# Performance work log

Measured on AMD Instinct MI355X. Metric: run time of the kernel, lower is better.

The kernel has to match this reference:

```python
import jax, jax.numpy as jnp
import numpy as np

B, N, FIN = 4, 4096, 128
H, U = 4, 32

def setup_inputs() -> dict:
    key = jax.random.key(0)
    k = jax.random.split(key, 6)
    x = jax.random.normal(k[0], (B, N, FIN), dtype=jnp.float32)
    adj = (jax.random.uniform(k[1], (B, N, N)) < 0.05).astype(jnp.float32)
    glorot = lambda kk, shape, fi, fo: jax.random.uniform(kk, shape, jnp.float32,
                                                          -np.sqrt(6.0/(fi+fo)), np.sqrt(6.0/(fi+fo)))
    W = glorot(k[2], (FIN, H*U), FIN, H*U)
    a_src = glorot(k[3], (H, U, 1), U, 1)
    a_dst = glorot(k[4], (H, U, 1), U, 1)
    bias = jnp.zeros((H*U,), dtype=jnp.float32)
    return {"x": x, "adj": adj, "W": W, "a_src": a_src, "a_dst": a_dst, "bias": bias}

def reference(x, adj, W, a_src, a_dst, bias):
    # inference mode: attention dropout is a no-op
    b, n, _ = x.shape
    h_heads, u = a_src.shape[0], a_src.shape[1]
    # add self-loops, clip to {0,1}
    adj = jnp.clip(adj + jnp.eye(n, dtype=adj.dtype)[None], 0.0, 1.0)
    h = (x @ W).reshape(b, n, h_heads, u).transpose(0, 2, 1, 3)      # [B,H,N,U]
    f1 = jnp.einsum('bhnu,hu->bhn', h, a_src[..., 0])                # [B,H,N]
    f2 = jnp.einsum('bhnu,hu->bhn', h, a_dst[..., 0])                # [B,H,N]
    e = f1[:, :, :, None] + f2[:, :, None, :]                        # [B,H,N,N]
    e = jnp.where(e > 0, e, 0.2 * e)                                 # LeakyReLU(0.2)
    e = jnp.where(adj[:, None] > 0.0, e, jnp.float32(-1e9))
    alpha = jax.nn.softmax(e, axis=-1)
    out = jnp.einsum('bhij,bhju->bhiu', alpha, h)                    # [B,H,N,U]
    out = out.transpose(0, 2, 1, 3).reshape(b, n, h_heads * u) + bias
    return jnp.where(out > 0, out, jnp.expm1(out))                   # ELU
```

## Files before the change

kernel.cpp:

```cpp
#include <hip/hip_runtime.h>
#include <math.h>

#define NB   4
#define NN   4096
#define FIN  128
#define FOUT 128
#define NH   4
#define UU   32

__device__ __forceinline__ unsigned short f2bf(float f) {
    unsigned u = __float_as_uint(f);
    u += 0x7fff + ((u >> 16) & 1);
    return (unsigned short)(u >> 16);
}

#define K1_ROWS 64
#define K1_RT   8
#define K1_CT   4
#define XPAD    132

__global__ __launch_bounds__(256) void k1_feat(
    const float* __restrict__ x, const float* __restrict__ W,
    const float* __restrict__ a_src, const float* __restrict__ a_dst,
    unsigned short* __restrict__ hbf, float* __restrict__ f1g, float* __restrict__ f2g)
{
    __shared__ __align__(16) float Wq[32 * FOUT];
    __shared__ __align__(16) float xs[K1_ROWS * XPAD];

    const int tid  = threadIdx.x;
    const int row0 = blockIdx.x * K1_ROWS;

    const float4* x4 = (const float4*)(x + (size_t)row0 * FIN);
    for (int idx = tid; idx < K1_ROWS * FIN / 4; idx += 256) {
        int r = idx >> 5, q = idx & 31;
        *(float4*)(xs + r * XPAD + q * 4) = x4[idx];
    }

    const int cg = tid & 31;
    const int rg = tid >> 5;
    float acc[K1_RT][K1_CT];
    #pragma unroll
    for (int rr = 0; rr < K1_RT; rr++)
        #pragma unroll
        for (int cc = 0; cc < K1_CT; cc++) acc[rr][cc] = 0.f;

    for (int kt = 0; kt < 4; kt++) {
        __syncthreads();
        for (int idx = tid; idx < 32 * FOUT / 4; idx += 256)
            ((float4*)Wq)[idx] = ((const float4*)W)[kt * 1024 + idx];
        __syncthreads();
        #pragma unroll
        for (int k4 = 0; k4 < 8; k4++) {
            const int kb = kt * 32 + k4 * 4;
            float4 xv[K1_RT];
            #pragma unroll
            for (int rr = 0; rr < K1_RT; rr++)
                xv[rr] = *(const float4*)(xs + (rg * K1_RT + rr) * XPAD + kb);
            #pragma unroll
            for (int kk = 0; kk < 4; kk++) {
                float wv[K1_CT];
                #pragma unroll
                for (int cc = 0; cc < K1_CT; cc++)
                    wv[cc] = Wq[(k4 * 4 + kk) * FOUT + cg + 32 * cc];
                #pragma unroll
                for (int rr = 0; rr < K1_RT; rr++) {
                    float xk = ((const float*)&xv[rr])[kk];
                    #pragma unroll
                    for (int cc = 0; cc < K1_CT; cc++)
                        acc[rr][cc] = fmaf(xk, wv[cc], acc[rr][cc]);
                }
            }
        }
    }
    __syncthreads();
    #pragma unroll
    for (int rr = 0; rr < K1_RT; rr++)
        #pragma unroll
        for (int cc = 0; cc < K1_CT; cc++)
            xs[(rg * K1_RT + rr) * XPAD + cg + 32 * cc] = acc[rr][cc];
    __syncthreads();

    unsigned short* hrow = hbf + (size_t)row0 * FOUT;
    for (int idx = tid; idx < K1_ROWS * FOUT / 8; idx += 256) {
        int r = idx >> 4, q = idx & 15;
        const float* src = xs + r * XPAD + q * 8;
        uint4 o;
        o.x = (unsigned)f2bf(src[0]) | ((unsigned)f2bf(src[1]) << 16);
        o.y = (unsigned)f2bf(src[2]) | ((unsigned)f2bf(src[3]) << 16);
        o.z = (unsigned)f2bf(src[4]) | ((unsigned)f2bf(src[5]) << 16);
        o.w = (unsigned)f2bf(src[6]) | ((unsigned)f2bf(src[7]) << 16);
        *(uint4*)(hrow + (size_t)r * FOUT + q * 8) = o;
    }

    for (int task = tid; task < K1_ROWS * NH * 2; task += 256) {
        int row = task >> 3;
        int head = (task >> 1) & 3;
        int which = task & 1;
        const float* av = which ? a_dst : a_src;
        float s = 0.f;
        #pragma unroll
        for (int u = 0; u < UU; u++)
            s += xs[row * XPAD + head * UU + u] * av[head * UU + u];
        float* dst = which ? f2g : f1g;
        dst[(size_t)(row0 + row) * NH + head] = s;
    }
}

#define CAP   512
#define APAD  516
#define PPART 132

__device__ __forceinline__ float lrelu(float e) { return e > 0.f ? e : 0.2f * e; }

__global__ __launch_bounds__(256) void k2_gat(
    const float* __restrict__ adj, const unsigned short* __restrict__ hbf,
    const float* __restrict__ f1g, const float* __restrict__ f2g,
    const float* __restrict__ bias, float* __restrict__ out)
{
    const int q    = blockIdx.x;
    const int xcd  = q & 7;
    const int b    = xcd >> 1;
    const int i    = ((q >> 3) << 1) | (xcd & 1);
    const int row  = b * NN + i;
    const int tid  = threadIdx.x;
    const int lane = tid & 63;
    const int wv   = tid >> 6;

    __shared__ int   nbr[CAP];
    __shared__ float alpha[NH][APAD];
    __shared__ float part[16][PPART];
    __shared__ float inv_s[NH];
    __shared__ int   wcnt[4];

    const float4* arow = (const float4*)(adj + (size_t)row * NN);
    float4 v[4];
    #pragma unroll
    for (int it = 0; it < 4; it++)
        v[it] = arow[wv * 256 + it * 64 + lane];

    const unsigned long long below = (1ull << lane) - 1ull;
    int my_cnt = 0;
    #pragma unroll
    for (int it = 0; it < 4; it++) {
        const int jb = (wv * 256 + it * 64 + lane) << 2;
        my_cnt += __popcll(__ballot((v[it].x > 0.f) | (jb + 0 == i)));
        my_cnt += __popcll(__ballot((v[it].y > 0.f) | (jb + 1 == i)));
        my_cnt += __popcll(__ballot((v[it].z > 0.f) | (jb + 2 == i)));
        my_cnt += __popcll(__ballot((v[it].w > 0.f) | (jb + 3 == i)));
    }
    if (lane == 0) wcnt[wv] = my_cnt;
    __syncthreads();

    const int w0 = wcnt[0], w1 = wcnt[1], w2 = wcnt[2], w3 = wcnt[3];
    int run = (wv > 0 ? w0 : 0) + (wv > 1 ? w1 : 0) + (wv > 2 ? w2 : 0);
    const int total = w0 + w1 + w2 + w3;
    const int K = (total < CAP) ? total : CAP;

    const float4* f2b = (const float4*)(f2g + (size_t)b * NN * NH);
    const float4  f1v = ((const float4*)f1g)[row];
    #pragma unroll
    for (int it = 0; it < 4; it++) {
        const int jb = (wv * 256 + it * 64 + lane) << 2;
        const bool p0 = (v[it].x > 0.f) | (jb + 0 == i);
        const bool p1 = (v[it].y > 0.f) | (jb + 1 == i);
        const bool p2 = (v[it].z > 0.f) | (jb + 2 == i);
        const bool p3 = (v[it].w > 0.f) | (jb + 3 == i);
        unsigned long long m0 = __ballot(p0), m1 = __ballot(p1);
        unsigned long long m2 = __ballot(p2), m3 = __ballot(p3);
        int c0 = __popcll(m0), c1 = __popcll(m1), c2 = __popcll(m2), c3 = __popcll(m3);
        #pragma unroll
        for (int e = 0; e < 4; e++) {
            bool pe = e == 0 ? p0 : e == 1 ? p1 : e == 2 ? p2 : p3;
            unsigned long long me = e == 0 ? m0 : e == 1 ? m1 : e == 2 ? m2 : m3;
            int pre = e == 0 ? 0 : e == 1 ? c0 : e == 2 ? c0 + c1 : c0 + c1 + c2;
            if (pe) {
                int p = run + pre + __popcll(me & below);
                if (p < CAP) {
                    int j = jb + e;
                    nbr[p] = j;
                    float4 f2v = f2b[j];
                    alpha[0][p] = lrelu(f1v.x + f2v.x);
                    alpha[1][p] = lrelu(f1v.y + f2v.y);
                    alpha[2][p] = lrelu(f1v.z + f2v.z);
                    alpha[3][p] = lrelu(f1v.w + f2v.w);
                }
            }
        }
        run += c0 + c1 + c2 + c3;
    }
    __syncthreads();

    {
        float m = -1e30f;
        for (int k = lane; k < K; k += 64) m = fmaxf(m, alpha[wv][k]);
        #pragma unroll
        for (int off = 32; off > 0; off >>= 1) m = fmaxf(m, __shfl_xor(m, off, 64));
        float s = 0.f;
        for (int k = lane; k < K; k += 64) {
            float a = __expf(alpha[wv][k] - m);
            alpha[wv][k] = a;
            s += a;
        }
        #pragma unroll
        for (int off = 32; off > 0; off >>= 1) s += __shfl_xor(s, off, 64);
        if (lane == 0) inv_s[wv] = 1.f / s;
    }
    __syncthreads();

    const int cq = tid & 15;
    const int kg = tid >> 4;
    const int hh = cq >> 2;
    const unsigned short* hb = hbf + (size_t)b * NN * FOUT + cq * 8;
    float acc[8];
    #pragma unroll
    for (int t = 0; t < 8; t++) acc[t] = 0.f;

    int k = kg;
    for (; k + 16 < K; k += 32) {
        int j0 = nbr[k], j1 = nbr[k + 16];
        float a0 = alpha[hh][k], a1 = alpha[hh][k + 16];
        uint4 u4a = *(const uint4*)(hb + (size_t)j0 * FOUT);
        uint4 u4b = *(const uint4*)(hb + (size_t)j1 * FOUT);
        const unsigned* u0 = (const unsigned*)&u4a;
        const unsigned* u1 = (const unsigned*)&u4b;
        #pragma unroll
        for (int t = 0; t < 4; t++) {
            acc[2*t]   = fmaf(a0, __uint_as_float(u0[t] << 16),          acc[2*t]);
            acc[2*t+1] = fmaf(a0, __uint_as_float(u0[t] & 0xffff0000u),  acc[2*t+1]);
        }
        #pragma unroll
        for (int t = 0; t < 4; t++) {
            acc[2*t]   = fmaf(a1, __uint_as_float(u1[t] << 16),          acc[2*t]);
            acc[2*t+1] = fmaf(a1, __uint_as_float(u1[t] & 0xffff0000u),  acc[2*t+1]);
        }
    }
    if (k < K) {
        int j0 = nbr[k];
        float a0 = alpha[hh][k];
        uint4 u4a = *(const uint4*)(hb + (size_t)j0 * FOUT);
        const unsigned* u0 = (const unsigned*)&u4a;
        #pragma unroll
        for (int t = 0; t < 4; t++) {
            acc[2*t]   = fmaf(a0, __uint_as_float(u0[t] << 16),          acc[2*t]);
            acc[2*t+1] = fmaf(a0, __uint_as_float(u0[t] & 0xffff0000u),  acc[2*t+1]);
        }
    }
    *(float4*)&part[kg][cq * 8]     = *(float4*)&acc[0];
    *(float4*)&part[kg][cq * 8 + 4] = *(float4*)&acc[4];
    __syncthreads();

    if (tid < FOUT) {
        float o = 0.f;
        #pragma unroll
        for (int g = 0; g < 16; g++) o += part[g][tid];
        o = o * inv_s[tid >> 5] + bias[tid];
        o = o > 0.f ? o : expm1f(o);
        out[(size_t)row * FOUT + tid] = o;
    }
}

extern "C" void kernel_launch(void* const* d_in, const int* in_sizes, int n_in,
                              void* d_out, int out_size, void* d_ws, size_t ws_size,
                              hipStream_t stream) {
    const float* x     = (const float*)d_in[0];
    const float* adj   = (const float*)d_in[1];
    const float* W     = (const float*)d_in[2];
    const float* a_src = (const float*)d_in[3];
    const float* a_dst = (const float*)d_in[4];
    const float* bias  = (const float*)d_in[5];
    float* out = (float*)d_out;

    char* ws = (char*)d_ws;
    unsigned short* hbf = (unsigned short*)ws;
    float* f1g = (float*)(ws + (size_t)NB * NN * FOUT * 2);
    float* f2g = f1g + (size_t)NB * NN * NH;

    k1_feat<<<NB * NN / K1_ROWS, 256, 0, stream>>>(x, W, a_src, a_dst, hbf, f1g, f2g);
    k2_gat<<<NB * NN, 256, 0, stream>>>(adj, hbf, f1g, f2g, bias, out);
}
```

Baseline: 427.6 us.

## Process eight rows per block with register prefetch of next adjacency row

The GAT aggregation kernel now has each block loop over eight rows, strided by 512, instead of handling one row. The next row's adjacency slice and f1 values are loaded into registers while the current row is being processed, so the large adjacency read overlaps with compute. The softmax is reorganised so all 256 threads score neighbours for all four heads at once using float4 values, with cross-wave max and sum reductions in shared memory. Barriers become raw s_barrier calls that wait only on LDS. The trade-offs are higher register pressure from the prefetch buffers and a grid that fills the device only once, leaving less block-level parallelism to hide latency.

```diff
diff --git a/kernel.cpp b/kernel.cpp
--- a/kernel.cpp
+++ b/kernel.cpp
@@ -13,6 +13,8 @@
     u += 0x7fff + ((u >> 16) & 1);
     return (unsigned short)(u >> 16);
 }
+
+#define LBAR() asm volatile("s_waitcnt lgkmcnt(0)\n\ts_barrier" ::: "memory")
 
 #define K1_ROWS 64
 #define K1_RT   8
@@ -107,155 +109,206 @@
 }
 
 #define CAP   512
-#define APAD  516
 #define PPART 132
+#define RPB   8
 
 __device__ __forceinline__ float lrelu(float e) { return e > 0.f ? e : 0.2f * e; }
 
-__global__ __launch_bounds__(256) void k2_gat(
+__global__ __launch_bounds__(256, 8) void k2_gat(
     const float* __restrict__ adj, const unsigned short* __restrict__ hbf,
     const float* __restrict__ f1g, const float* __restrict__ f2g,
     const float* __restrict__ bias, float* __restrict__ out)
 {
-    const int q    = blockIdx.x;
-    const int xcd  = q & 7;
+    const int p    = blockIdx.x;
+    const int xcd  = p & 7;
     const int b    = xcd >> 1;
-    const int i    = ((q >> 3) << 1) | (xcd & 1);
-    const int row  = b * NN + i;
+    const int l    = ((p >> 3) << 1) | (p & 1);
     const int tid  = threadIdx.x;
     const int lane = tid & 63;
     const int wv   = tid >> 6;
 
-    __shared__ int   nbr[CAP];
-    __shared__ float alpha[NH][APAD];
-    __shared__ float part[16][PPART];
-    __shared__ float inv_s[NH];
-    __shared__ int   wcnt[4];
-
-    const float4* arow = (const float4*)(adj + (size_t)row * NN);
-    float4 v[4];
-    #pragma unroll
-    for (int it = 0; it < 4; it++)
-        v[it] = arow[wv * 256 + it * 64 + lane];
-
+    __shared__ int    nbr[CAP];
+    __shared__ __align__(16) float4 alpha4[CAP];
+    __shared__ float  part[16][PPART];
+    __shared__ __align__(16) float4 smax4[4];
+    __shared__ float  wsum[16];
+    __shared__ int    wcnt[4];
+
+    const float4* f2b = (const float4*)(f2g + (size_t)b * NN * NH);
+    const unsigned short* hbase = hbf + (size_t)b * NN * FOUT;
     const unsigned long long below = (1ull << lane) - 1ull;
-    int my_cnt = 0;
-    #pragma unroll
-    for (int it = 0; it < 4; it++) {
-        const int jb = (wv * 256 + it * 64 + lane) << 2;
-        my_cnt += __popcll(__ballot((v[it].x > 0.f) | (jb + 0 == i)));
-        my_cnt += __popcll(__ballot((v[it].y > 0.f) | (jb + 1 == i)));
-        my_cnt += __popcll(__ballot((v[it].z > 0.f) | (jb + 2 == i)));
-        my_cnt += __popcll(__ballot((v[it].w > 0.f) | (jb + 3 == i)));
-    }
-    if (lane == 0) wcnt[wv] = my_cnt;
-    __syncthreads();
-
-    const int w0 = wcnt[0], w1 = wcnt[1], w2 = wcnt[2], w3 = wcnt[3];
-    int run = (wv > 0 ? w0 : 0) + (wv > 1 ? w1 : 0) + (wv > 2 ? w2 : 0);
-    const int total = w0 + w1 + w2 + w3;
-    const int K = (total < CAP) ? total : CAP;
-
-    const float4* f2b = (const float4*)(f2g + (size_t)b * NN * NH);
-    const float4  f1v = ((const float4*)f1g)[row];
-    #pragma unroll
-    for (int it = 0; it < 4; it++) {
-        const int jb = (wv * 256 + it * 64 + lane) << 2;
-        const bool p0 = (v[it].x > 0.f) | (jb + 0 == i);
-        const bool p1 = (v[it].y > 0.f) | (jb + 1 == i);
-        const bool p2 = (v[it].z > 0.f) | (jb + 2 == i);
-        const bool p3 = (v[it].w > 0.f) | (jb + 3 == i);
-        unsigned long long m0 = __ballot(p0), m1 = __ballot(p1);
-        unsigned long long m2 = __ballot(p2), m3 = __ballot(p3);
-        int c0 = __popcll(m0), c1 = __popcll(m1), c2 = __popcll(m2), c3 = __popcll(m3);
-        #pragma unroll
-        for (int e = 0; e < 4; e++) {
-            bool pe = e == 0 ? p0 : e == 1 ? p1 : e == 2 ? p2 : p3;
-            unsigned long long me = e == 0 ? m0 : e == 1 ? m1 : e == 2 ? m2 : m3;
-            int pre = e == 0 ? 0 : e == 1 ? c0 : e == 2 ? c0 + c1 : c0 + c1 + c2;
-            if (pe) {
-                int p = run + pre + __popcll(me & below);
-                if (p < CAP) {
-                    int j = jb + e;
-                    nbr[p] = j;
-                    float4 f2v = f2b[j];
-                    alpha[0][p] = lrelu(f1v.x + f2v.x);
-                    alpha[1][p] = lrelu(f1v.y + f2v.y);
-                    alpha[2][p] = lrelu(f1v.z + f2v.z);
-                    alpha[3][p] = lrelu(f1v.w + f2v.w);
-                }
+
+    const int cq = tid & 15, kg = tid >> 4, hh = cq >> 2;
+    const unsigned short* hb = hbase + cq * 8;
+    const float bias_r = (tid < FOUT) ? bias[tid] : 0.f;
+
+    int i = l;
+    float4 v[4], vn[4], f1v, f1n;
+    {
+        const float4* arow = (const float4*)(adj + (size_t)(b * NN + i) * NN);
+        #pragma unroll
+        for (int it = 0; it < 4; it++) v[it] = arow[wv * 256 + it * 64 + lane];
+        f1v = ((const float4*)f1g)[b * NN + i];
+    }
+
+    for (int t = 0; t < RPB; t++) {
+        const int row = b * NN + i;
+
+        int my_cnt = 0;
+        #pragma unroll
+        for (int it = 0; it < 4; it++) {
+            const int jb = ((it * 4 + wv) * 64 + lane) << 2;
+        }
+        #pragma unroll
+        for (int it = 0; it < 4; it++) {
+            const int jb = (wv * 256 + it * 64 + lane) << 2;
+            my_cnt += __popcll(__ballot((v[it].x > 0.f) | (jb + 0 == i)));
+            my_cnt += __popcll(__ballot((v[it].y > 0.f) | (jb + 1 == i)));
+            my_cnt += __popcll(__ballot((v[it].z > 0.f) | (jb + 2 == i)));
+            my_cnt += __popcll(__ballot((v[it].w > 0.f) | (jb + 3 == i)));
+        }
+        if (lane == 0) wcnt[wv] = my_cnt;
+        LBAR();
+
+        const int w0 = wcnt[0], w1 = wcnt[1], w2 = wcnt[2], w3 = wcnt[3];
+        int run = (wv > 0 ? w0 : 0) + (wv > 1 ? w1 : 0) + (wv > 2 ? w2 : 0);
+        const int total = w0 + w1 + w2 + w3;
+        const int K = (total < CAP) ? total : CAP;
+
+        #pragma unroll
+        for (int it = 0; it < 4; it++) {
+            const int jb = (wv * 256 + it * 64 + lane) << 2;
+            const bool p0 = (v[it].x > 0.f) | (jb + 0 == i);
+            const bool p1 = (v[it].y > 0.f) | (jb + 1 == i);
+            const bool p2 = (v[it].z > 0.f) | (jb + 2 == i);
+            const bool p3 = (v[it].w > 0.f) | (jb + 3 == i);
+            unsigned long long m0 = __ballot(p0), m1 = __ballot(p1);
+            unsigned long long m2 = __ballot(p2), m3 = __ballot(p3);
+            int c0 = __popcll(m0), c1 = __popcll(m1), c2 = __popcll(m2), c3 = __popcll(m3);
+            if (p0) { int s = run + __popcll(m0 & below);                if (s < CAP) nbr[s] = jb + 0; }
+            if (p1) { int s = run + c0 + __popcll(m1 & below);           if (s < CAP) nbr[s] = jb + 1; }
+            if (p2) { int s = run + c0 + c1 + __popcll(m2 & below);      if (s < CAP) nbr[s] = jb + 2; }
+            if (p3) { int s = run + c0 + c1 + c2 + __popcll(m3 & below); if (s < CAP) nbr[s] = jb + 3; }
+            run += c0 + c1 + c2 + c3;
+        }
+
+        if (t + 1 < RPB) {
+            const int inext = i + 512;
+            const float4* arowN = (const float4*)(adj + (size_t)(b * NN + inext) * NN);
+            #pragma unroll
+            for (int it = 0; it < 4; it++) vn[it] = arowN[wv * 256 + it * 64 + lane];
+            f1n = ((const float4*)f1g)[b * NN + inext];
+        }
+        LBAR();
+
+        float4 hmax = make_float4(-1e30f, -1e30f, -1e30f, -1e30f);
+        for (int k = tid; k < K; k += 256) {
+            int j = nbr[k];
+            float4 f2v = f2b[j];
+            float4 e;
+            e.x = lrelu(f1v.x + f2v.x);
+            e.y = lrelu(f1v.y + f2v.y);
+            e.z = lrelu(f1v.z + f2v.z);
+            e.w = lrelu(f1v.w + f2v.w);
+            alpha4[k] = e;
+            hmax.x = fmaxf(hmax.x, e.x); hmax.y = fmaxf(hmax.y, e.y);
+            hmax.z = fmaxf(hmax.z, e.z); hmax.w = fmaxf(hmax.w, e.w);
+        }
+        #pragma unroll
+        for (int off = 32; off > 0; off >>= 1) {
+            hmax.x = fmaxf(hmax.x, __shfl_xor(hmax.x, off, 64));
+            hmax.y = fmaxf(hmax.y, __shfl_xor(hmax.y, off, 64));
+            hmax.z = fmaxf(hmax.z, __shfl_xor(hmax.z, off, 64));
+            hmax.w = fmaxf(hmax.w, __shfl_xor(hmax.w, off, 64));
+        }
+        if (lane == 0) smax4[wv] = hmax;
+        LBAR();
+
+        float4 g0 = smax4[0], g1 = smax4[1], g2 = smax4[2], g3 = smax4[3];
+        float4 gmax;
+        gmax.x = fmaxf(fmaxf(g0.x, g1.x), fmaxf(g2.x, g3.x));
+        gmax.y = fmaxf(fmaxf(g0.y, g1.y), fmaxf(g2.y, g3.y));
+        gmax.z = fmaxf(fmaxf(g0.z, g1.z), fmaxf(g2.z, g3.z));
+        gmax.w = fmaxf(fmaxf(g0.w, g1.w), fmaxf(g2.w, g3.w));
+        float4 hsum = make_float4(0.f, 0.f, 0.f, 0.f);
+        for (int k = tid; k < K; k += 256) {
+            float4 e = alpha4[k];
+            e.x = __expf(e.x - gmax.x);
+            e.y = __expf(e.y - gmax.y);
+            e.z = __expf(e.z - gmax.z);
+            e.w = __expf(e.w - gmax.w);
+            alpha4[k] = e;
+            hsum.x += e.x; hsum.y += e.y; hsum.z += e.z; hsum.w += e.w;
+        }
+        #pragma unroll
+        for (int off = 32; off > 0; off >>= 1) {
+            hsum.x += __shfl_xor(hsum.x, off, 64);
+            hsum.y += __shfl_xor(hsum.y, off, 64);
+            hsum.z += __shfl_xor(hsum.z, off, 64);
+            hsum.w += __shfl_xor(hsum.w, off, 64);
+        }
+        if (lane == 0) {
+            wsum[wv * 4 + 0] = hsum.x; wsum[wv * 4 + 1] = hsum.y;
+            wsum[wv * 4 + 2] = hsum.z; wsum[wv * 4 + 3] = hsum.w;
+        }
+        LBAR();
+
+        const float* alpf = (const float*)alpha4;
+        float acc[8];
+        #pragma unroll
+        for (int u = 0; u < 8; u++) acc[u] = 0.f;
+        int k = kg;
+        for (; k + 16 < K; k += 32) {
+            int j0 = nbr[k], j1 = nbr[k + 16];
+            float a0 = alpf[k * 4 + hh], a1 = alpf[(k + 16) * 4 + hh];
+            uint4 u4a = *(const uint4*)(hb + (size_t)j0 * FOUT);
+            uint4 u4b = *(const uint4*)(hb + (size_t)j1 * FOUT);
+            const unsigned* u0 = (const unsigned*)&u4a;
+            const unsigned* u1 = (const unsigned*)&u4b;
+            #pragma unroll
+            for (int u = 0; u < 4; u++) {
+                acc[2*u]   = fmaf(a0, __uint_as_float(u0[u] << 16),         acc[2*u]);
+                acc[2*u+1] = fmaf(a0, __uint_as_float(u0[u] & 0xffff0000u), acc[2*u+1]);
             }
-        }
-        run += c0 + c1 + c2 + c3;
-    }
-    __syncthreads();
-
-    {
-        float m = -1e30f;
-        for (int k = lane; k < K; k += 64) m = fmaxf(m, alpha[wv][k]);
-        #pragma unroll
-        for (int off = 32; off > 0; off >>= 1) m = fmaxf(m, __shfl_xor(m, off, 64));
-        float s = 0.f;
-        for (int k = lane; k < K; k += 64) {
-            float a = __expf(alpha[wv][k] - m);
-            alpha[wv][k] = a;
-            s += a;
-        }
-        #pragma unroll
-        for (int off = 32; off > 0; off >>= 1) s += __shfl_xor(s, off, 64);
-        if (lane == 0) inv_s[wv] = 1.f / s;
-    }
-    __syncthreads();
-
-    const int cq = tid & 15;
-    const int kg = tid >> 4;
-    const int hh = cq >> 2;
-    const unsigned short* hb = hbf + (size_t)b * NN * FOUT + cq * 8;
-    float acc[8];
-    #pragma unroll
-    for (int t = 0; t < 8; t++) acc[t] = 0.f;
-
-    int k = kg;
-    for (; k + 16 < K; k += 32) {
-        int j0 = nbr[k], j1 = nbr[k + 16];
-        float a0 = alpha[hh][k], a1 = alpha[hh][k + 16];
-        uint4 u4a = *(const uint4*)(hb + (size_t)j0 * FOUT);
-        uint4 u4b = *(const uint4*)(hb + (size_t)j1 * FOUT);
-        const unsigned* u0 = (const unsigned*)&u4a;
-        const unsigned* u1 = (const unsigned*)&u4b;
-        #pragma unroll
-        for (int t = 0; t < 4; t++) {
-            acc[2*t]   = fmaf(a0, __uint_as_float(u0[t] << 16),          acc[2*t]);
-            acc[2*t+1] = fmaf(a0, __uint_as_float(u0[t] & 0xffff0000u),  acc[2*t+1]);
-        }
-        #pragma unroll
-        for (int t = 0; t < 4; t++) {
-            acc[2*t]   = fmaf(a1, __uint_as_float(u1[t] << 16),          acc[2*t]);
-            acc[2*t+1] = fmaf(a1, __uint_as_float(u1[t] & 0xffff0000u),  acc[2*t+1]);
-        }
-    }
-    if (k < K) {
-        int j0 = nbr[k];
-        float a0 = alpha[hh][k];
-        uint4 u4a = *(const uint4*)(hb + (size_t)j0 * FOUT);
-        const unsigned* u0 = (const unsigned*)&u4a;
-        #pragma unroll
-        for (int t = 0; t < 4; t++) {
-            acc[2*t]   = fmaf(a0, __uint_as_float(u0[t] << 16),          acc[2*t]);
-            acc[2*t+1] = fmaf(a0, __uint_as_float(u0[t] & 0xffff0000u),  acc[2*t+1]);
-        }
-    }
-    *(float4*)&part[kg][cq * 8]     = *(float4*)&acc[0];
-    *(float4*)&part[kg][cq * 8 + 4] = *(float4*)&acc[4];
-    __syncthreads();
-
-    if (tid < FOUT) {
-        float o = 0.f;
-        #pragma unroll
-        for (int g = 0; g < 16; g++) o += part[g][tid];
-        o = o * inv_s[tid >> 5] + bias[tid];
-        o = o > 0.f ? o : expm1f(o);
-        out[(size_t)row * FOUT + tid] = o;
+            #pragma unroll
+            for (int u = 0; u < 4; u++) {
+                acc[2*u]   = fmaf(a1, __uint_as_float(u1[u] << 16),         acc[2*u]);
+                acc[2*u+1] = fmaf(a1, __uint_as_float(u1[u] & 0xffff0000u), acc[2*u+1]);
+            }
+        }
+        if (k < K) {
+            int j0 = nbr[k];
+            float a0 = alpf[k * 4 + hh];
+            uint4 u4a = *(const uint4*)(hb + (size_t)j0 * FOUT);
+            const unsigned* u0 = (const unsigned*)&u4a;
+            #pragma unroll
+            for (int u = 0; u < 4; u++) {
+                acc[2*u]   = fmaf(a0, __uint_as_float(u0[u] << 16),         acc[2*u]);
+                acc[2*u+1] = fmaf(a0, __uint_as_float(u0[u] & 0xffff0000u), acc[2*u+1]);
+            }
+        }
+        *(float4*)&part[kg][cq * 8]     = *(float4*)&acc[0];
+        *(float4*)&part[kg][cq * 8 + 4] = *(float4*)&acc[4];
+        LBAR();
+
+        if (tid < FOUT) {
+            const int h = tid >> 5;
+            float s = wsum[h] + wsum[4 + h] + wsum[8 + h] + wsum[12 + h];
+            float o = 0.f;
+            #pragma unroll
+            for (int g = 0; g < 16; g++) o += part[g][tid];
+            o = o / s + bias_r;
+            o = o > 0.f ? o : expm1f(o);
+            out[(size_t)row * FOUT + tid] = o;
+        }
+        LBAR();
+
+        if (t + 1 < RPB) {
+            #pragma unroll
+            for (int it = 0; it < 4; it++) v[it] = vn[it];
+            f1v = f1n;
+            i += 512;
+        }
     }
 }
 
@@ -276,5 +329,5 @@
     float* f2g = f1g + (size_t)NB * NN * NH;
 
     k1_feat<<<NB * NN / K1_ROWS, 256, 0, stream>>>(x, W, a_src, a_dst, hbf, f1g, f2g);
-    k2_gat<<<NB * NN, 256, 0, stream>>>(adj, hbf, f1g, f2g, bias, out);
+    k2_gat<<<NB * NN / RPB, 256, 0, stream>>>(adj, hbf, f1g, f2g, bias, out);
 }
```

Result: slower. 517.2 us (+21.0%).
